# Optimization experiments

Hardware: AMD Instinct MI355X
Metric: run time of the kernel (lower is better)

Reference implementation:

```python
import jax, jax.numpy as jnp
import numpy as np
from jax.ops import segment_sum

N_NODES = 100000


def _add_self_loops(edge_index, n):
    loop = jnp.arange(n, dtype=edge_index.dtype)
    src = jnp.concatenate([edge_index[0], loop])
    dst = jnp.concatenate([edge_index[1], loop])
    return src, dst


def _gcn_conv(x, W, b, src, dst, n):
    # PyG GCNConv: h = X W; out[i] = sum_j norm(j,i) h[j] + b, with self-loops
    h = x @ W                                             # [N, out]
    deg = segment_sum(jnp.ones_like(src, dtype=x.dtype), dst, num_segments=n)
    dinv = jnp.where(deg > 0, jax.lax.rsqrt(deg), 0.0)    # deg^{-1/2}
    norm = dinv[src] * dinv[dst]                          # [E]
    msg = h[src] * norm[:, None]                          # gather + scale
    out = segment_sum(msg, dst, num_segments=n)           # scatter-add
    return out + b


def setup_inputs() -> dict:
    key = jax.random.key(0)
    ks = jax.random.split(key, 8)
    x = jax.random.normal(ks[0], (N_NODES, 128), dtype=jnp.float32)
    edge_index = jax.random.randint(ks[1], (2, 600000), 0, N_NODES, dtype=jnp.int64)
    s1 = 1.0 / np.sqrt(128); s2 = 1.0 / np.sqrt(64); s3 = 1.0 / np.sqrt(32)
    return {
        "x": x,
        "edge_index": edge_index,
        "W1": jax.random.uniform(ks[2], (128, 64), jnp.float32, -s1, s1),
        "b1": jnp.zeros((64,), jnp.float32),
        "W2": jax.random.uniform(ks[3], (64, 32), jnp.float32, -s2, s2),
        "b2": jnp.zeros((32,), jnp.float32),
        "Wc": jax.random.uniform(ks[4], (32, 1), jnp.float32, -s3, s3),
        "bc": jnp.zeros((1,), jnp.float32),
    }


def reference(x, edge_index, W1, b1, W2, b2, Wc, bc):
    n = x.shape[0]
    src, dst = _add_self_loops(edge_index, n)
    h = jax.nn.relu(_gcn_conv(x, W1, b1, src, dst, n))
    h = jax.nn.relu(_gcn_conv(h, W2, b2, src, dst, n))
    return h @ Wc + bc
```

## Files before the change

kernel.cpp:

```cpp
#include <hip/hip_runtime.h>


#define SCAN_THREADS 256
#define SCAN_PER_T   8
#define SCAN_TILE    (SCAN_THREADS * SCAN_PER_T)

__global__ __launch_bounds__(256) void count_kernel(const int* __restrict__ dst,
                                                    int* __restrict__ deg, int E) {
    int e = blockIdx.x * blockDim.x + threadIdx.x;
    if (e < E) atomicAdd(&deg[dst[e]], 1);
}

__global__ __launch_bounds__(SCAN_THREADS) void tile_reduce_kernel(const int* __restrict__ deg,
                                                                   int* __restrict__ bsum,
                                                                   int n) {
    __shared__ int s[SCAN_THREADS];
    int t = threadIdx.x;
    int gbase = blockIdx.x * SCAN_TILE + t * SCAN_PER_T;
    int local = 0;
#pragma unroll
    for (int k = 0; k < SCAN_PER_T; ++k) {
        int i = gbase + k;
        if (i < n) local += deg[i];
    }
    s[t] = local;
    __syncthreads();
    for (int off = SCAN_THREADS / 2; off > 0; off >>= 1) {
        if (t < off) s[t] += s[t + off];
        __syncthreads();
    }
    if (t == 0) bsum[blockIdx.x] = s[0];
}

__global__ __launch_bounds__(SCAN_THREADS) void scan_bsums_kernel(int* __restrict__ bsum,
                                                                  int* __restrict__ row_ptr,
                                                                  int nb, int n) {
    __shared__ int s[SCAN_THREADS];
    int t = threadIdx.x;
    s[t] = (t < nb) ? bsum[t] : 0;
    __syncthreads();
    for (int off = 1; off < SCAN_THREADS; off <<= 1) {
        int v = (t >= off) ? s[t - off] : 0;
        __syncthreads();
        s[t] += v;
        __syncthreads();
    }
    if (t < nb) bsum[t] = (t == 0) ? 0 : s[t - 1];
    if (t == 0) row_ptr[n] = s[nb - 1];
}

__global__ __launch_bounds__(SCAN_THREADS) void tile_apply_kernel(int* __restrict__ deg,
                                                                  const int* __restrict__ bsum,
                                                                  int* __restrict__ row_ptr,
                                                                  float* __restrict__ dinv,
                                                                  int n) {
    __shared__ int s[SCAN_THREADS];
    int t = threadIdx.x;
    int gbase = blockIdx.x * SCAN_TILE + t * SCAN_PER_T;

    int d[SCAN_PER_T];
    int inc[SCAN_PER_T];
    int run = 0;
#pragma unroll
    for (int k = 0; k < SCAN_PER_T; ++k) {
        int i = gbase + k;
        d[k] = (i < n) ? deg[i] : 0;
        run += d[k];
        inc[k] = run;
    }
    s[t] = run;
    __syncthreads();
    for (int off = 1; off < SCAN_THREADS; off <<= 1) {
        int v = (t >= off) ? s[t - off] : 0;
        __syncthreads();
        s[t] += v;
        __syncthreads();
    }
    int base = bsum[blockIdx.x] + ((t == 0) ? 0 : s[t - 1]);
#pragma unroll
    for (int k = 0; k < SCAN_PER_T; ++k) {
        int i = gbase + k;
        if (i < n) {
            int ex = base + inc[k] - d[k];
            row_ptr[i] = ex;
            deg[i] = ex;
            dinv[i] = rsqrtf((float)(d[k] + 1));
        }
    }
}

__global__ __launch_bounds__(256) void fill_kernel(const int* __restrict__ src,
                                                   const int* __restrict__ dst,
                                                   int* __restrict__ cursor,
                                                   int* __restrict__ col, int E) {
    int e = blockIdx.x * blockDim.x + threadIdx.x;
    if (e < E) {
        int pos = atomicAdd(&cursor[dst[e]], 1);
        col[pos] = src[e];
    }
}

template <int IN, int OUT, int BM, int TM, int TN>
__global__ __launch_bounds__(256) void gemm_tiled(const float* __restrict__ X,
                                                  const float* __restrict__ W,
                                                  const float* __restrict__ dinv,
                                                  float* __restrict__ H, int n) {
    constexpr int BK = 32;
    constexpr int S = 132;
    constexpr int NTX = OUT / TN;
    constexpr int NKT = IN / BK;
    static_assert(NTX * (BM / TM) == 256, "thread mapping");

    __shared__ float Ws[IN * OUT];
    __shared__ float Xs[2][BK * S];

    const int t = threadIdx.x;
    for (int i = t; i < IN * OUT / 4; i += 256)
        ((float4*)Ws)[i] = ((const float4*)W)[i];

    const int node0 = blockIdx.x * BM;
    const int tx = t % NTX;
    const int ty = t / NTX;
    const int row0 = ty * TM;
    const int jb = tx * TN;

    const int snd = t >> 3;
    const int skq = t & 7;

    float acc[TM][TN];
#pragma unroll
    for (int i = 0; i < TM; ++i)
#pragma unroll
        for (int j = 0; j < TN; ++j) acc[i][j] = 0.f;

    float4 stgA[4], stgB[4];
#pragma unroll
    for (int i = 0; i < 4; ++i) {
        int nd = snd + 32 * i;
        stgA[i] = make_float4(0.f, 0.f, 0.f, 0.f);
        if (node0 + nd < n)
            stgA[i] = *(const float4*)(X + (size_t)(node0 + nd) * IN + skq * 4);
    }
    if (NKT > 1) {
#pragma unroll
        for (int i = 0; i < 4; ++i) {
            int nd = snd + 32 * i;
            stgB[i] = make_float4(0.f, 0.f, 0.f, 0.f);
            if (node0 + nd < n)
                stgB[i] = *(const float4*)(X + (size_t)(node0 + nd) * IN + BK + skq * 4);
        }
    }

    int cur = 0;
    for (int kt = 0; kt < NKT; ++kt) {
#pragma unroll
        for (int i = 0; i < 4; ++i) {
            int nd = snd + 32 * i;
            float* p = Xs[cur] + (skq * 4) * S + nd;
            float4 v = (kt & 1) ? stgB[i] : stgA[i];
            p[0 * S] = v.x; p[1 * S] = v.y; p[2 * S] = v.z; p[3 * S] = v.w;
        }
        __syncthreads();

        if (kt + 2 < NKT) {
#pragma unroll
            for (int i = 0; i < 4; ++i) {
                int nd = snd + 32 * i;
                float4 v = make_float4(0.f, 0.f, 0.f, 0.f);
                if (node0 + nd < n)
                    v = *(const float4*)(X + (size_t)(node0 + nd) * IN +
                                         (kt + 2) * BK + skq * 4);
                if (kt & 1) stgB[i] = v; else stgA[i] = v;
            }
        }

        const float* xb = Xs[cur];
        const float* wb = Ws + (size_t)kt * BK * OUT + jb;
#pragma unroll 4
        for (int k = 0; k < BK; ++k) {
            float4 wv = *(const float4*)(wb + (size_t)k * OUT);
            float xv[TM];
#pragma unroll
            for (int i4 = 0; i4 < TM; i4 += 4) {
                float4 xq = *(const float4*)(xb + k * S + row0 + i4);
                xv[i4 + 0] = xq.x; xv[i4 + 1] = xq.y;
                xv[i4 + 2] = xq.z; xv[i4 + 3] = xq.w;
            }
#pragma unroll
            for (int i = 0; i < TM; ++i) {
                acc[i][0] += xv[i] * wv.x;
                acc[i][1] += xv[i] * wv.y;
                acc[i][2] += xv[i] * wv.z;
                acc[i][3] += xv[i] * wv.w;
            }
        }
        __syncthreads();
        cur ^= 1;
    }

#pragma unroll
    for (int i = 0; i < TM; ++i) {
        int node = node0 + row0 + i;
        if (node < n) {
            float di = dinv[node];
            *(float4*)(H + (size_t)node * OUT + jb) =
                make_float4(di * acc[i][0], di * acc[i][1],
                            di * acc[i][2], di * acc[i][3]);
        }
    }
}

template <int F>
__global__ __launch_bounds__(256) void agg_relu_kernel(const int* __restrict__ row_ptr,
                                                       const int* __restrict__ col,
                                                       const float* __restrict__ dinv,
                                                       const float* __restrict__ H,
                                                       const float* __restrict__ b,
                                                       float* __restrict__ OUT, int n) {
    constexpr int TPE = F / 4;
    int t = blockIdx.x * blockDim.x + threadIdx.x;
    int node = t / TPE;
    int c = t % TPE;
    if (node >= n) return;
    int rs = row_ptr[node], re = row_ptr[node + 1];
    float4 acc = make_float4(0.f, 0.f, 0.f, 0.f);
    int e = rs;
    for (; e + 3 < re; e += 4) {
        int s0 = col[e], s1 = col[e + 1], s2 = col[e + 2], s3 = col[e + 3];
        float4 v0 = *(const float4*)(H + (size_t)s0 * F + c * 4);
        float4 v1 = *(const float4*)(H + (size_t)s1 * F + c * 4);
        float4 v2 = *(const float4*)(H + (size_t)s2 * F + c * 4);
        float4 v3 = *(const float4*)(H + (size_t)s3 * F + c * 4);
        acc.x += (v0.x + v1.x) + (v2.x + v3.x);
        acc.y += (v0.y + v1.y) + (v2.y + v3.y);
        acc.z += (v0.z + v1.z) + (v2.z + v3.z);
        acc.w += (v0.w + v1.w) + (v2.w + v3.w);
    }
    for (; e < re; ++e) {
        int s0 = col[e];
        float4 v0 = *(const float4*)(H + (size_t)s0 * F + c * 4);
        acc.x += v0.x; acc.y += v0.y; acc.z += v0.z; acc.w += v0.w;
    }
    float di = dinv[node];
    float4 hs = *(const float4*)(H + (size_t)node * F + c * 4);
    float4 bb = *(const float4*)(b + c * 4);
    float4 r;
    r.x = di * (acc.x + hs.x) + bb.x;
    r.y = di * (acc.y + hs.y) + bb.y;
    r.z = di * (acc.z + hs.z) + bb.z;
    r.w = di * (acc.w + hs.w) + bb.w;
    r.x = r.x > 0.f ? r.x : 0.f;
    r.y = r.y > 0.f ? r.y : 0.f;
    r.z = r.z > 0.f ? r.z : 0.f;
    r.w = r.w > 0.f ? r.w : 0.f;
    *(float4*)(OUT + (size_t)node * F + c * 4) = r;
}

__global__ __launch_bounds__(256) void agg_final_kernel(const int* __restrict__ row_ptr,
                                                        const int* __restrict__ col,
                                                        const float* __restrict__ dinv,
                                                        const float* __restrict__ H,
                                                        const float* __restrict__ b2,
                                                        const float* __restrict__ Wc,
                                                        const float* __restrict__ bc,
                                                        float* __restrict__ out, int n) {
    constexpr int F = 32, TPE = 8;
    int t = blockIdx.x * blockDim.x + threadIdx.x;
    int node = t / TPE;
    int c = t % TPE;
    if (node >= n) return;
    int rs = row_ptr[node], re = row_ptr[node + 1];
    float4 acc = make_float4(0.f, 0.f, 0.f, 0.f);
    int e = rs;
    for (; e + 3 < re; e += 4) {
        int s0 = col[e], s1 = col[e + 1], s2 = col[e + 2], s3 = col[e + 3];
        float4 v0 = *(const float4*)(H + (size_t)s0 * F + c * 4);
        float4 v1 = *(const float4*)(H + (size_t)s1 * F + c * 4);
        float4 v2 = *(const float4*)(H + (size_t)s2 * F + c * 4);
        float4 v3 = *(const float4*)(H + (size_t)s3 * F + c * 4);
        acc.x += (v0.x + v1.x) + (v2.x + v3.x);
        acc.y += (v0.y + v1.y) + (v2.y + v3.y);
        acc.z += (v0.z + v1.z) + (v2.z + v3.z);
        acc.w += (v0.w + v1.w) + (v2.w + v3.w);
    }
    for (; e < re; ++e) {
        int s0 = col[e];
        float4 v0 = *(const float4*)(H + (size_t)s0 * F + c * 4);
        acc.x += v0.x; acc.y += v0.y; acc.z += v0.z; acc.w += v0.w;
    }
    float di = dinv[node];
    float4 hs = *(const float4*)(H + (size_t)node * F + c * 4);
    float4 bb = *(const float4*)(b2 + c * 4);
    float4 wc = *(const float4*)(Wc + c * 4);
    float4 r;
    r.x = di * (acc.x + hs.x) + bb.x;
    r.y = di * (acc.y + hs.y) + bb.y;
    r.z = di * (acc.z + hs.z) + bb.z;
    r.w = di * (acc.w + hs.w) + bb.w;
    float dot = (r.x > 0.f ? r.x : 0.f) * wc.x + (r.y > 0.f ? r.y : 0.f) * wc.y +
                (r.z > 0.f ? r.z : 0.f) * wc.z + (r.w > 0.f ? r.w : 0.f) * wc.w;
    dot += __shfl_xor(dot, 1, 8);
    dot += __shfl_xor(dot, 2, 8);
    dot += __shfl_xor(dot, 4, 8);
    if (c == 0) out[node] = dot + bc[0];
}

extern "C" void kernel_launch(void* const* d_in, const int* in_sizes, int n_in,
                              void* d_out, int out_size, void* d_ws, size_t ws_size,
                              hipStream_t stream) {
    const float* x  = (const float*)d_in[0];
    const int*   ei = (const int*)d_in[1];
    const float* W1 = (const float*)d_in[2];
    const float* b1 = (const float*)d_in[3];
    const float* W2 = (const float*)d_in[4];
    const float* b2 = (const float*)d_in[5];
    const float* Wc = (const float*)d_in[6];
    const float* bc = (const float*)d_in[7];
    float* out = (float*)d_out;

    const int n = in_sizes[0] / 128;
    const int E = in_sizes[1] / 2;

    const int* src = ei;
    const int* dst = ei + (size_t)E;

    const int nb = (n + SCAN_TILE - 1) / SCAN_TILE;

    float* dinv    = (float*)d_ws;
    int*   deg     = (int*)d_ws + n;
    int*   row_ptr = (int*)d_ws + 2 * (size_t)n;
    int*   col     = row_ptr + (n + 1);
    int*   bsum    = col + E;
    float* bufA    = (float*)(bsum + 256);
    float* bufB    = bufA + (size_t)n * 64;

    hipMemsetAsync(deg, 0, (size_t)n * 4, stream);
    count_kernel<<<(E + 255) / 256, 256, 0, stream>>>(dst, deg, E);
    tile_reduce_kernel<<<nb, SCAN_THREADS, 0, stream>>>(deg, bsum, n);
    scan_bsums_kernel<<<1, SCAN_THREADS, 0, stream>>>(bsum, row_ptr, nb, n);
    tile_apply_kernel<<<nb, SCAN_THREADS, 0, stream>>>(deg, bsum, row_ptr, dinv, n);
    fill_kernel<<<(E + 255) / 256, 256, 0, stream>>>(src, dst, deg, col, E);

    const int gemm_grid = (n + 127) / 128;

    gemm_tiled<128, 64, 128, 8, 4><<<gemm_grid, 256, 0, stream>>>(x, W1, dinv, bufA, n);
    agg_relu_kernel<64><<<(n * 16 + 255) / 256, 256, 0, stream>>>(row_ptr, col, dinv,
                                                                  bufA, b1, bufB, n);
    gemm_tiled<64, 32, 128, 4, 4><<<gemm_grid, 256, 0, stream>>>(bufB, W2, dinv, bufA, n);
    agg_final_kernel<<<(n * 8 + 255) / 256, 256, 0, stream>>>(row_ptr, col, dinv,
                                                              bufA, b2, Wc, bc, out, n);
}
```

Before: 266.5 us.

## Split first GEMM output columns across grid.y and restructure X double-buffering

```diff
diff --git a/kernel.cpp b/kernel.cpp
--- a/kernel.cpp
+++ b/kernel.cpp
@@ -100,23 +100,27 @@
     }
 }
 
-template <int IN, int OUT, int BM, int TM, int TN>
+template <int IN, int OUT, int OSL, int BM, int TM, int TN>
 __global__ __launch_bounds__(256) void gemm_tiled(const float* __restrict__ X,
                                                   const float* __restrict__ W,
                                                   const float* __restrict__ dinv,
                                                   float* __restrict__ H, int n) {
     constexpr int BK = 32;
     constexpr int S = 132;
-    constexpr int NTX = OUT / TN;
+    constexpr int NTX = OSL / TN;
     constexpr int NKT = IN / BK;
     static_assert(NTX * (BM / TM) == 256, "thread mapping");
 
-    __shared__ float Ws[IN * OUT];
+    __shared__ float Ws[IN * OSL];
     __shared__ float Xs[2][BK * S];
 
     const int t = threadIdx.x;
-    for (int i = t; i < IN * OUT / 4; i += 256)
-        ((float4*)Ws)[i] = ((const float4*)W)[i];
+    const int jb0 = blockIdx.y * OSL;
+    for (int f = t; f < IN * OSL / 4; f += 256) {
+        int row = f / (OSL / 4);
+        int q = f % (OSL / 4);
+        ((float4*)Ws)[f] = *(const float4*)(W + (size_t)row * OUT + jb0 + q * 4);
+    }
 
     const int node0 = blockIdx.x * BM;
     const int tx = t % NTX;
@@ -133,52 +137,59 @@
 #pragma unroll
         for (int j = 0; j < TN; ++j) acc[i][j] = 0.f;
 
-    float4 stgA[4], stgB[4];
+    float4 stg[4];
 #pragma unroll
     for (int i = 0; i < 4; ++i) {
         int nd = snd + 32 * i;
-        stgA[i] = make_float4(0.f, 0.f, 0.f, 0.f);
+        stg[i] = make_float4(0.f, 0.f, 0.f, 0.f);
         if (node0 + nd < n)
-            stgA[i] = *(const float4*)(X + (size_t)(node0 + nd) * IN + skq * 4);
+            stg[i] = *(const float4*)(X + (size_t)(node0 + nd) * IN + skq * 4);
+    }
+#pragma unroll
+    for (int i = 0; i < 4; ++i) {
+        int nd = snd + 32 * i;
+        float* p = Xs[0] + (skq * 4) * S + nd;
+        p[0 * S] = stg[i].x; p[1 * S] = stg[i].y;
+        p[2 * S] = stg[i].z; p[3 * S] = stg[i].w;
     }
     if (NKT > 1) {
 #pragma unroll
         for (int i = 0; i < 4; ++i) {
             int nd = snd + 32 * i;
-            stgB[i] = make_float4(0.f, 0.f, 0.f, 0.f);
+            stg[i] = make_float4(0.f, 0.f, 0.f, 0.f);
             if (node0 + nd < n)
-                stgB[i] = *(const float4*)(X + (size_t)(node0 + nd) * IN + BK + skq * 4);
+                stg[i] = *(const float4*)(X + (size_t)(node0 + nd) * IN + BK + skq * 4);
         }
     }
 
     int cur = 0;
     for (int kt = 0; kt < NKT; ++kt) {
-#pragma unroll
-        for (int i = 0; i < 4; ++i) {
-            int nd = snd + 32 * i;
-            float* p = Xs[cur] + (skq * 4) * S + nd;
-            float4 v = (kt & 1) ? stgB[i] : stgA[i];
-            p[0 * S] = v.x; p[1 * S] = v.y; p[2 * S] = v.z; p[3 * S] = v.w;
-        }
-        __syncthreads();
-
-        if (kt + 2 < NKT) {
+        __syncthreads();
+        if (kt + 1 < NKT) {
 #pragma unroll
             for (int i = 0; i < 4; ++i) {
                 int nd = snd + 32 * i;
-                float4 v = make_float4(0.f, 0.f, 0.f, 0.f);
+                float* p = Xs[cur ^ 1] + (skq * 4) * S + nd;
+                p[0 * S] = stg[i].x; p[1 * S] = stg[i].y;
+                p[2 * S] = stg[i].z; p[3 * S] = stg[i].w;
+            }
+        }
+        if (kt + 2 < NKT) {
+#pragma unroll
+            for (int i = 0; i < 4; ++i) {
+                int nd = snd + 32 * i;
+                stg[i] = make_float4(0.f, 0.f, 0.f, 0.f);
                 if (node0 + nd < n)
-                    v = *(const float4*)(X + (size_t)(node0 + nd) * IN +
-                                         (kt + 2) * BK + skq * 4);
-                if (kt & 1) stgB[i] = v; else stgA[i] = v;
+                    stg[i] = *(const float4*)(X + (size_t)(node0 + nd) * IN +
+                                              (kt + 2) * BK + skq * 4);
             }
         }
 
         const float* xb = Xs[cur];
-        const float* wb = Ws + (size_t)kt * BK * OUT + jb;
+        const float* wb = Ws + (size_t)kt * BK * OSL + jb;
 #pragma unroll 4
         for (int k = 0; k < BK; ++k) {
-            float4 wv = *(const float4*)(wb + (size_t)k * OUT);
+            float4 wv = *(const float4*)(wb + (size_t)k * OSL);
             float xv[TM];
 #pragma unroll
             for (int i4 = 0; i4 < TM; i4 += 4) {
@@ -194,7 +205,6 @@
                 acc[i][3] += xv[i] * wv.w;
             }
         }
-        __syncthreads();
         cur ^= 1;
     }
 
@@ -203,7 +213,7 @@
         int node = node0 + row0 + i;
         if (node < n) {
             float di = dinv[node];
-            *(float4*)(H + (size_t)node * OUT + jb) =
+            *(float4*)(H + (size_t)node * OUT + jb0 + jb) =
                 make_float4(di * acc[i][0], di * acc[i][1],
                             di * acc[i][2], di * acc[i][3]);
         }
@@ -341,12 +351,18 @@
     tile_apply_kernel<<<nb, SCAN_THREADS, 0, stream>>>(deg, bsum, row_ptr, dinv, n);
     fill_kernel<<<(E + 255) / 256, 256, 0, stream>>>(src, dst, deg, col, E);
 
-    const int gemm_grid = (n + 127) / 128;
-
-    gemm_tiled<128, 64, 128, 8, 4><<<gemm_grid, 256, 0, stream>>>(x, W1, dinv, bufA, n);
+    const int gemm_bx = (n + 127) / 128;
+
+    {
+        dim3 grid(gemm_bx, 2);
+        gemm_tiled<128, 64, 32, 128, 4, 4><<<grid, 256, 0, stream>>>(x, W1, dinv, bufA, n);
+    }
     agg_relu_kernel<64><<<(n * 16 + 255) / 256, 256, 0, stream>>>(row_ptr, col, dinv,
                                                                   bufA, b1, bufB, n);
-    gemm_tiled<64, 32, 128, 4, 4><<<gemm_grid, 256, 0, stream>>>(bufB, W2, dinv, bufA, n);
+    {
+        dim3 grid(gemm_bx, 1);
+        gemm_tiled<64, 32, 32, 128, 4, 4><<<grid, 256, 0, stream>>>(bufB, W2, dinv, bufA, n);
+    }
     agg_final_kernel<<<(n * 8 + 255) / 256, 256, 0, stream>>>(row_ptr, col, dinv,
                                                               bufA, b2, Wc, bc, out, n);
 }
```

Result: no change. 266.5 us (+0.0%).
